# Kernel optimization log

Hardware: AMD Instinct MI355X
Metric: run time of the kernel (lower is better)

## Reference

```python
import jax, jax.numpy as jnp
import numpy as np

B, S, D = 2, 2048, 1024
H = 16
HD = D // H  # 64
THETA = 10000.0


def apply_rope(x, positions, theta):
    # x: (b, h, s, hd); positions: (s,)
    hd = x.shape[-1]
    inv_freq = theta ** (-jnp.arange(0, hd, 2, dtype=jnp.float32) / hd)  # (hd/2,)
    angles = positions.astype(jnp.float32)[:, None] * inv_freq[None, :]  # (s, hd/2)
    cos, sin = jnp.cos(angles), jnp.sin(angles)
    x1 = x[..., 0::2]
    x2 = x[..., 1::2]
    r1 = x1 * cos - x2 * sin
    r2 = x1 * sin + x2 * cos
    out = jnp.stack([r1, r2], axis=-1).reshape(x.shape)
    return out.astype(x.dtype)


def setup_inputs() -> dict:
    key = jax.random.key(0)
    ks = jax.random.split(key, 5)
    scale = 1.0 / np.sqrt(D)
    return {
        "in_features": jax.random.normal(ks[0], (B, S, D), dtype=jnp.float32),
        "token_positions": jnp.arange(S, dtype=jnp.int32),
        "Wq": jax.random.normal(ks[1], (D, D), dtype=jnp.float32) * scale,
        "Wk": jax.random.normal(ks[2], (D, D), dtype=jnp.float32) * scale,
        "Wv": jax.random.normal(ks[3], (D, D), dtype=jnp.float32) * scale,
        "Wo": jax.random.normal(ks[4], (D, D), dtype=jnp.float32) * scale,
    }


def reference(in_features, token_positions, Wq, Wk, Wv, Wo):
    b, s, d = in_features.shape
    h, hd = H, HD
    # bias-free linear: y = x @ W.T  (W is (out, in))
    q = in_features @ Wq.T
    k = in_features @ Wk.T
    v = in_features @ Wv.T
    # (b, s, h*hd) -> (b, h, s, hd)
    split = lambda t: t.reshape(b, s, h, hd).transpose(0, 2, 1, 3)
    q, k, v = split(q), split(k), split(v)
    q = apply_rope(q, token_positions, THETA)
    k = apply_rope(k, token_positions, THETA)
    scores = jnp.einsum("bhid,bhjd->bhij", q, k) / jnp.sqrt(jnp.asarray(hd, dtype=q.dtype))
    causal = jnp.triu(jnp.ones((s, s), dtype=bool), k=1)
    scores = jnp.where(causal, -jnp.inf, scores)
    attn = jax.nn.softmax(scores, axis=-1)
    out = jnp.einsum("bhij,bhjd->bhid", attn, v)
    out = out.transpose(0, 2, 1, 3).reshape(b, s, d)
    return out @ Wo.T
```

## Files before the change

kernel.cpp:

```cpp
#include <hip/hip_runtime.h>
#include <math.h>

#define NUM_HEADS 16
#define HEAD_DIM 64

typedef __bf16 bf16x8 __attribute__((ext_vector_type(8)));
typedef short shortx4 __attribute__((ext_vector_type(4)));
typedef float floatx4 __attribute__((ext_vector_type(4)));

__device__ __forceinline__ unsigned short f2b(float f) {
  unsigned int u = __float_as_uint(f);
  u += 0x7fffu + ((u >> 16) & 1u);
  return (unsigned short)(u >> 16);
}

__device__ __forceinline__ void async16(const void* g, void* l) {
  __builtin_amdgcn_global_load_lds(
      (const __attribute__((address_space(1))) unsigned int*)g,
      (__attribute__((address_space(3))) unsigned int*)l, 16, 0, 0);
}

__device__ __forceinline__ void cvt4(const float* in, unsigned short* out, int i) {
  float4 v = ((const float4*)in)[i];
  ushort4 o;
  o.x = f2b(v.x); o.y = f2b(v.y); o.z = f2b(v.z); o.w = f2b(v.w);
  ((ushort4*)out)[i] = o;
}

__global__ void prep(const float* __restrict__ x,
                     const float* __restrict__ w0, const float* __restrict__ w1,
                     const float* __restrict__ w2, const float* __restrict__ w3,
                     const int* __restrict__ pos,
                     unsigned short* Xb, unsigned short* o0, unsigned short* o1,
                     unsigned short* o2, unsigned short* o3,
                     float* __restrict__ tab, int xq, int w4, int ntab) {
  int i = blockIdx.x * 256 + threadIdx.x;
  int z = blockIdx.y;
  if (z == 0) {
    if (i < xq) {
#pragma unroll
      for (int rep = 0; rep < 4; ++rep) cvt4(x, Xb, rep * xq + i);
    }
  } else if (z <= 4) {
    if (i < w4) {
      const float* in = (z == 1) ? w0 : (z == 2) ? w1 : (z == 3) ? w2 : w3;
      unsigned short* out = (z == 1) ? o0 : (z == 2) ? o1 : (z == 3) ? o2 : o3;
      cvt4(in, out, i);
    }
  } else {
    if (i < ntab) {
      int fi = i & 31, s = i >> 5;
      float inv = expf(-0.28782313662425575f * (float)fi);
      float ang = (float)pos[s] * inv;
      float sn, cs;
      sincosf(ang, &sn, &cs);
      tab[i * 2] = cs;
      tab[i * 2 + 1] = sn;
    }
  }
}

template <int MODE, int MT>
__global__ __launch_bounds__(256, MODE == 1 ? 4 : 2)
void gemm_bt(const unsigned short* __restrict__ A,
             const unsigned short* __restrict__ B0,
             const unsigned short* __restrict__ B1,
             const unsigned short* __restrict__ B2,
             void* out0v, void* out1v, void* out2v,
             const float* __restrict__ ctab,
             int M, int N, int K, int S) {
  __shared__ unsigned short As[(MT / 16) * 512];
  __shared__ unsigned short Bs[8 * 512];
  const int tid = threadIdx.x;
  const int lane = tid & 63;
  const int w = tid >> 6;
  const int lane16 = lane & 15;
  const int g = lane >> 4;
  const int wm = w >> 1, wn = w & 1;
  const int m0 = blockIdx.y * MT;
  const int n0 = blockIdx.x * 128;
  const unsigned short* Bp = (blockIdx.z == 0) ? B0 : (blockIdx.z == 1 ? B1 : B2);
  constexpr int MTILES = MT / 32;

  const floatx4 vzero = {0.f, 0.f, 0.f, 0.f};
  floatx4 acc[MTILES][4];
#pragma unroll
  for (int i = 0; i < MTILES; i++)
#pragma unroll
    for (int j = 0; j < 4; j++) acc[i][j] = vzero;

  const int ar = lane >> 2;
  const int ac = (lane & 3) * 8;

  for (int k0 = 0; k0 < K; k0 += 32) {
    if constexpr (MT == 128) {
#pragma unroll
      for (int c = 0; c < 2; c++) {
        int chunk = w * 2 + c;
        async16(A  + (size_t)(m0 + chunk * 16 + ar) * K + k0 + ac, As + chunk * 512);
        async16(Bp + (size_t)(n0 + chunk * 16 + ar) * K + k0 + ac, Bs + chunk * 512);
      }
    } else {
      async16(A  + (size_t)(m0 + w * 16 + ar) * K + k0 + ac, As + w * 512);
      async16(Bp + (size_t)(n0 + w * 16 + ar) * K + k0 + ac, Bs + w * 512);
      async16(Bp + (size_t)(n0 + (w + 4) * 16 + ar) * K + k0 + ac, Bs + (w + 4) * 512);
    }
    __syncthreads();
    bf16x8 a[MTILES], b[4];
#pragma unroll
    for (int mt = 0; mt < MTILES; mt++)
      a[mt] = *(const bf16x8*)&As[(wm * (MT / 2) + mt * 16 + lane16) * 32 + g * 8];
#pragma unroll
    for (int nt = 0; nt < 4; nt++)
      b[nt] = *(const bf16x8*)&Bs[(wn * 64 + nt * 16 + lane16) * 32 + g * 8];
#pragma unroll
    for (int mt = 0; mt < MTILES; mt++)
#pragma unroll
      for (int nt = 0; nt < 4; nt++)
        acc[mt][nt] = __builtin_amdgcn_mfma_f32_16x16x32_bf16(b[nt], a[mt], acc[mt][nt], 0, 0, 0);
    __syncthreads();
  }

  if (MODE == 0) {
    if (blockIdx.z < 2) {
      unsigned short* outp = (unsigned short*)((blockIdx.z == 0) ? out0v : out1v);
      const float qs = (blockIdx.z == 0) ? 0.125f : 1.0f;
#pragma unroll
      for (int mt = 0; mt < MTILES; mt++) {
        int m = m0 + wm * (MT / 2) + mt * 16 + lane16;
        int bb = m / S, s = m - bb * S;
        const float* crow = ctab + (size_t)s * 64;
#pragma unroll
        for (int nt = 0; nt < 4; nt++) {
          int n = n0 + wn * 64 + nt * 16 + g * 4;
          int h = n >> 6, dl = n & 63;
          floatx4 v = acc[mt][nt];
          float4 cs = *(const float4*)&crow[dl];
          float r0 = (v[0] * cs.x - v[1] * cs.y) * qs;
          float r1 = (v[0] * cs.y + v[1] * cs.x) * qs;
          float r2 = (v[2] * cs.z - v[3] * cs.w) * qs;
          float r3 = (v[2] * cs.w + v[3] * cs.z) * qs;
          shortx4 st;
          st[0] = (short)f2b(r0); st[1] = (short)f2b(r1);
          st[2] = (short)f2b(r2); st[3] = (short)f2b(r3);
          *(shortx4*)&outp[(((size_t)(bb * NUM_HEADS + h) * S + s) << 6) + dl] = st;
        }
      }
    } else {
      unsigned short* outp = (unsigned short*)out2v;
#pragma unroll
      for (int mt = 0; mt < MTILES; mt++) {
        int m = m0 + wm * (MT / 2) + mt * 16 + lane16;
        int bb = m / S, s = m - bb * S;
#pragma unroll
        for (int nt = 0; nt < 4; nt++) {
          int n = n0 + wn * 64 + nt * 16 + g * 4;
          int bh = bb * NUM_HEADS + (n >> 6);
          int dl = n & 63;
          size_t dbase = ((size_t)bh * 64 + dl) * S + s;
#pragma unroll
          for (int r = 0; r < 4; r++)
            outp[dbase + (size_t)r * S] = f2b(acc[mt][nt][r]);
        }
      }
    }
  } else {
    float* outp = (float*)out0v;
#pragma unroll
    for (int mt = 0; mt < MTILES; mt++) {
      int m = m0 + wm * (MT / 2) + mt * 16 + lane16;
#pragma unroll
      for (int nt = 0; nt < 4; nt++) {
        int n = n0 + wn * 64 + nt * 16 + g * 4;
        *(floatx4*)&outp[(size_t)m * N + n] = acc[mt][nt];
      }
    }
  }
}

__global__ __launch_bounds__(256, 4)
void flash_attn4(const unsigned short* __restrict__ Q,
                 const unsigned short* __restrict__ Kv,
                 const unsigned short* __restrict__ Vt,
                 unsigned short* __restrict__ Oattn, int S) {
  __shared__ unsigned short Ks[2 * 4096];
  __shared__ unsigned short Vs[2 * 4096];
  const int tid = threadIdx.x;
  const int lane = tid & 63;
  const int w = tid >> 6;
  const int lane16 = lane & 15;
  const int g = lane >> 4;
  const int sw = lane16 & 7;
  const int qt = gridDim.x - 1 - blockIdx.x;
  const int bh = blockIdx.y;
  const int b = bh >> 4, h = bh & 15;
  const size_t kbase = (size_t)bh * S * HEAD_DIM;
  const unsigned short* Kbase = Kv + kbase;
  const unsigned short* Vtbase = Vt + (size_t)bh * HEAD_DIM * S;
  const int qrow0 = qt * 64 + w * 16;

  bf16x8 qf0, qf1;
  {
    const unsigned short* qp = Q + kbase + (size_t)(qrow0 + lane16) * HEAD_DIM + g * 8;
    qf0 = *(const bf16x8*)qp;
    qf1 = *(const bf16x8*)(qp + 32);
  }

  const int ci0 = w * 64 + lane;
  const int ci1 = ci0 + 256;
  const int r0 = ci0 >> 3, j0 = (ci0 & 7) ^ (r0 & 7);
  const int r1 = ci1 >> 3, j1 = (ci1 & 7) ^ (r1 & 7);
  const unsigned short* kS0 = Kbase + r0 * HEAD_DIM + j0 * 8;
  const unsigned short* kS1 = Kbase + r1 * HEAD_DIM + j1 * 8;
  const unsigned short* vS0 = Vtbase + (size_t)r0 * S + j0 * 8;
  const unsigned short* vS1 = Vtbase + (size_t)r1 * S + j1 * 8;
  unsigned short* kD0 = Ks + ci0 * 8;
  unsigned short* kD1 = Ks + ci1 * 8;
  unsigned short* vD0 = Vs + ci0 * 8;
  unsigned short* vD1 = Vs + ci1 * 8;

  auto stage = [&](int t, int bi) {
    int koff = t * 4096;
    int voff = t * 64;
    int doff = bi * 4096;
    async16(kS0 + koff, kD0 + doff);
    async16(kS1 + koff, kD1 + doff);
    async16(vS0 + voff, vD0 + doff);
    async16(vS1 + voff, vD1 + doff);
  };

  const floatx4 vzero = {0.f, 0.f, 0.f, 0.f};
  floatx4 oacc[4];
#pragma unroll
  for (int i = 0; i < 4; i++) oacc[i] = vzero;
  float l_i = 0.f;

  stage(0, 0);
  __syncthreads();

  for (int t = 0; t <= qt; ++t) {
    const int bi = t & 1;
    if (t < qt) stage(t + 1, bi ^ 1);
    const unsigned short* Kb_ = Ks + bi * 4096;
    const unsigned short* Vb_ = Vs + bi * 4096;

    floatx4 sc[4];
#pragma unroll
    for (int c = 0; c < 4; ++c) {
      int r = c * 16 + lane16;
      bf16x8 kf0 = *(const bf16x8*)&Kb_[(r * 8 + (g ^ sw)) * 8];
      bf16x8 kf1 = *(const bf16x8*)&Kb_[(r * 8 + ((4 + g) ^ sw)) * 8];
      floatx4 s = vzero;
      s = __builtin_amdgcn_mfma_f32_16x16x32_bf16(kf0, qf0, s, 0, 0, 0);
      s = __builtin_amdgcn_mfma_f32_16x16x32_bf16(kf1, qf1, s, 0, 0, 0);
      sc[c] = s;
    }
    if (t == qt) {
      const int i = qrow0 + lane16;
      const int jb = t * 64;
#pragma unroll
      for (int c = 0; c < 4; ++c)
#pragma unroll
        for (int r = 0; r < 4; ++r)
          if (jb + c * 16 + g * 4 + r > i) sc[c][r] = -INFINITY;
    }
    shortx4 pc[4];
#pragma unroll
    for (int c = 0; c < 4; ++c) {
      float p0 = __expf(sc[c][0]);
      float p1 = __expf(sc[c][1]);
      float p2 = __expf(sc[c][2]);
      float p3 = __expf(sc[c][3]);
      l_i += (p0 + p1) + (p2 + p3);
      union { unsigned int u[2]; shortx4 s4; } pu;
      pu.u[0] = __builtin_amdgcn_perm(__float_as_uint(p1), __float_as_uint(p0), 0x07060302u);
      pu.u[1] = __builtin_amdgcn_perm(__float_as_uint(p3), __float_as_uint(p2), 0x07060302u);
      pc[c] = pu.s4;
    }
#pragma unroll
    for (int nt = 0; nt < 4; ++nt) {
      int rv = nt * 16 + lane16;
#pragma unroll
      for (int c = 0; c < 4; ++c) {
        shortx4 vf = *(const shortx4*)&Vb_[(rv * 8 + ((c * 2 + (g >> 1)) ^ sw)) * 8 + (g & 1) * 4];
        oacc[nt] = __builtin_amdgcn_mfma_f32_16x16x16bf16_1k(vf, pc[c], oacc[nt], 0, 0, 0);
      }
    }
    __syncthreads();
  }

  l_i += __shfl_xor(l_i, 16, 64);
  l_i += __shfl_xor(l_i, 32, 64);
  {
    float inv = 1.0f / l_i;
    int srow = qrow0 + lane16;
    size_t rowb = ((size_t)b * S + srow) * 1024 + h * 64;
#pragma unroll
    for (int nt = 0; nt < 4; ++nt) {
      shortx4 st;
#pragma unroll
      for (int r = 0; r < 4; ++r) st[r] = (short)f2b(oacc[nt][r] * inv);
      *(shortx4*)&Oattn[rowb + nt * 16 + g * 4] = st;
    }
  }
}

extern "C" void kernel_launch(void* const* d_in, const int* in_sizes, int n_in,
                              void* d_out, int out_size, void* d_ws, size_t ws_size,
                              hipStream_t stream) {
  const float* x  = (const float*)d_in[0];
  const int*  pos = (const int*)d_in[1];
  const float* wq = (const float*)d_in[2];
  const float* wk = (const float*)d_in[3];
  const float* wv = (const float*)d_in[4];
  const float* wo = (const float*)d_in[5];

  const int D = 1024;
  const int S = in_sizes[1];
  const int M = in_sizes[0] / D;
  const int B = M / S;
  const int BH = B * NUM_HEADS;

  char* wsb = (char*)d_ws;
  size_t off = 0;
  auto alloc = [&](size_t bytes) {
    char* p = wsb + off;
    off += (bytes + 255) & ~(size_t)255;
    return p;
  };
  unsigned short* Xb   = (unsigned short*)alloc((size_t)M * D * 2);
  unsigned short* Wqb  = (unsigned short*)alloc((size_t)D * D * 2);
  unsigned short* Wkb  = (unsigned short*)alloc((size_t)D * D * 2);
  unsigned short* Wvb  = (unsigned short*)alloc((size_t)D * D * 2);
  unsigned short* Wob  = (unsigned short*)alloc((size_t)D * D * 2);
  unsigned short* Qb   = (unsigned short*)alloc((size_t)M * D * 2);
  unsigned short* Kb   = (unsigned short*)alloc((size_t)M * D * 2);
  unsigned short* Vtb  = (unsigned short*)alloc((size_t)M * D * 2);
  unsigned short* Attn = (unsigned short*)alloc((size_t)M * D * 2);
  float*          Ctab = (float*)alloc((size_t)S * 32 * 2 * 4);
  (void)ws_size;

  {
    int n4x = M * D / 4;
    int xq = n4x / 4;
    int w4 = D * D / 4;
    int ntab = S * 32;
    int gx = (w4 + 255) / 256;
    prep<<<dim3(gx, 6), 256, 0, stream>>>(x, wq, wk, wv, wo, pos,
                                          Xb, Wqb, Wkb, Wvb, Wob, Ctab,
                                          xq, w4, ntab);
  }
  gemm_bt<0, 128><<<dim3(D / 128, M / 128, 3), 256, 0, stream>>>(
      Xb, Wqb, Wkb, Wvb, Qb, Kb, Vtb, Ctab, M, D, D, S);
  flash_attn4<<<dim3(S / 64, BH), 256, 0, stream>>>(Qb, Kb, Vtb, Attn, S);
  gemm_bt<1, 64><<<dim3(D / 128, M / 64, 1), 256, 0, stream>>>(
      Attn, Wob, Wob, Wob, d_out, d_out, d_out, Ctab, M, D, D, S);
}
```

Baseline: 191.3 us.

## Pair complementary causal query tiles per block and use exp2 with folded scale

Each attention block now processes two query tiles, qa and NT-1-qa, sharing staged K/V tiles, which halves the grid and balances causal work across blocks. The softmax exponent switches to exp2, with log2(e) folded into the Q projection scale. Register pressure rises because two sets of accumulators are live, and launch bounds drop to 2 blocks per CU to allow for that.

```diff
diff --git a/kernel.cpp b/kernel.cpp
--- a/kernel.cpp
+++ b/kernel.cpp
@@ -7,6 +7,12 @@
 typedef __bf16 bf16x8 __attribute__((ext_vector_type(8)));
 typedef short shortx4 __attribute__((ext_vector_type(4)));
 typedef float floatx4 __attribute__((ext_vector_type(4)));
+
+#if __has_builtin(__builtin_amdgcn_exp2f)
+#define EXP2(x) __builtin_amdgcn_exp2f(x)
+#else
+#define EXP2(x) exp2f(x)
+#endif
 
 __device__ __forceinline__ unsigned short f2b(float f) {
   unsigned int u = __float_as_uint(f);
@@ -124,7 +130,7 @@
   if (MODE == 0) {
     if (blockIdx.z < 2) {
       unsigned short* outp = (unsigned short*)((blockIdx.z == 0) ? out0v : out1v);
-      const float qs = (blockIdx.z == 0) ? 0.125f : 1.0f;
+      const float qs = (blockIdx.z == 0) ? 0.18033688011112042f : 1.0f;
 #pragma unroll
       for (int mt = 0; mt < MTILES; mt++) {
         int m = m0 + wm * (MT / 2) + mt * 16 + lane16;
@@ -178,8 +184,8 @@
   }
 }
 
-__global__ __launch_bounds__(256, 4)
-void flash_attn4(const unsigned short* __restrict__ Q,
+__global__ __launch_bounds__(256, 2)
+void flash_attn5(const unsigned short* __restrict__ Q,
                  const unsigned short* __restrict__ Kv,
                  const unsigned short* __restrict__ Vt,
                  unsigned short* __restrict__ Oattn, int S) {
@@ -191,19 +197,25 @@
   const int lane16 = lane & 15;
   const int g = lane >> 4;
   const int sw = lane16 & 7;
-  const int qt = gridDim.x - 1 - blockIdx.x;
+  const int NT = S >> 6;
+  const int qa = blockIdx.x;
+  const int qb = NT - 1 - qa;
   const int bh = blockIdx.y;
   const int b = bh >> 4, h = bh & 15;
   const size_t kbase = (size_t)bh * S * HEAD_DIM;
   const unsigned short* Kbase = Kv + kbase;
   const unsigned short* Vtbase = Vt + (size_t)bh * HEAD_DIM * S;
-  const int qrow0 = qt * 64 + w * 16;
-
-  bf16x8 qf0, qf1;
+  const int qrowA = qa * 64 + w * 16;
+  const int qrowB = qb * 64 + w * 16;
+
+  bf16x8 qA0, qA1, qB0, qB1;
   {
-    const unsigned short* qp = Q + kbase + (size_t)(qrow0 + lane16) * HEAD_DIM + g * 8;
-    qf0 = *(const bf16x8*)qp;
-    qf1 = *(const bf16x8*)(qp + 32);
+    const unsigned short* qp = Q + kbase + (size_t)(qrowA + lane16) * HEAD_DIM + g * 8;
+    qA0 = *(const bf16x8*)qp;
+    qA1 = *(const bf16x8*)(qp + 32);
+    qp = Q + kbase + (size_t)(qrowB + lane16) * HEAD_DIM + g * 8;
+    qB0 = *(const bf16x8*)qp;
+    qB1 = *(const bf16x8*)(qp + 32);
   }
 
   const int ci0 = w * 64 + lane;
@@ -230,76 +242,141 @@
   };
 
   const floatx4 vzero = {0.f, 0.f, 0.f, 0.f};
-  floatx4 oacc[4];
-#pragma unroll
-  for (int i = 0; i < 4; i++) oacc[i] = vzero;
-  float l_i = 0.f;
+  floatx4 oA[4], oB[4];
+#pragma unroll
+  for (int i = 0; i < 4; i++) { oA[i] = vzero; oB[i] = vzero; }
+  float lA = 0.f, lB = 0.f;
 
   stage(0, 0);
   __syncthreads();
 
-  for (int t = 0; t <= qt; ++t) {
+  for (int t = 0; t <= qb; ++t) {
     const int bi = t & 1;
-    if (t < qt) stage(t + 1, bi ^ 1);
+    if (t < qb) stage(t + 1, bi ^ 1);
     const unsigned short* Kb_ = Ks + bi * 4096;
     const unsigned short* Vb_ = Vs + bi * 4096;
-
-    floatx4 sc[4];
+    const bool doA = (t <= qa);
+
+    bf16x8 kf0[4], kf1[4];
 #pragma unroll
     for (int c = 0; c < 4; ++c) {
       int r = c * 16 + lane16;
-      bf16x8 kf0 = *(const bf16x8*)&Kb_[(r * 8 + (g ^ sw)) * 8];
-      bf16x8 kf1 = *(const bf16x8*)&Kb_[(r * 8 + ((4 + g) ^ sw)) * 8];
+      kf0[c] = *(const bf16x8*)&Kb_[(r * 8 + (g ^ sw)) * 8];
+      kf1[c] = *(const bf16x8*)&Kb_[(r * 8 + ((4 + g) ^ sw)) * 8];
+    }
+
+    floatx4 scB[4];
+#pragma unroll
+    for (int c = 0; c < 4; ++c) {
       floatx4 s = vzero;
-      s = __builtin_amdgcn_mfma_f32_16x16x32_bf16(kf0, qf0, s, 0, 0, 0);
-      s = __builtin_amdgcn_mfma_f32_16x16x32_bf16(kf1, qf1, s, 0, 0, 0);
-      sc[c] = s;
-    }
-    if (t == qt) {
-      const int i = qrow0 + lane16;
+      s = __builtin_amdgcn_mfma_f32_16x16x32_bf16(kf0[c], qB0, s, 0, 0, 0);
+      s = __builtin_amdgcn_mfma_f32_16x16x32_bf16(kf1[c], qB1, s, 0, 0, 0);
+      scB[c] = s;
+    }
+    if (t == qb) {
+      const int i = qrowB + lane16;
       const int jb = t * 64;
 #pragma unroll
       for (int c = 0; c < 4; ++c)
 #pragma unroll
         for (int r = 0; r < 4; ++r)
-          if (jb + c * 16 + g * 4 + r > i) sc[c][r] = -INFINITY;
-    }
-    shortx4 pc[4];
+          if (jb + c * 16 + g * 4 + r > i) scB[c][r] = -INFINITY;
+    }
+    shortx4 pcB[4], pcA[4];
 #pragma unroll
     for (int c = 0; c < 4; ++c) {
-      float p0 = __expf(sc[c][0]);
-      float p1 = __expf(sc[c][1]);
-      float p2 = __expf(sc[c][2]);
-      float p3 = __expf(sc[c][3]);
-      l_i += (p0 + p1) + (p2 + p3);
+      float p0 = EXP2(scB[c][0]);
+      float p1 = EXP2(scB[c][1]);
+      float p2 = EXP2(scB[c][2]);
+      float p3 = EXP2(scB[c][3]);
+      lB += (p0 + p1) + (p2 + p3);
       union { unsigned int u[2]; shortx4 s4; } pu;
       pu.u[0] = __builtin_amdgcn_perm(__float_as_uint(p1), __float_as_uint(p0), 0x07060302u);
       pu.u[1] = __builtin_amdgcn_perm(__float_as_uint(p3), __float_as_uint(p2), 0x07060302u);
-      pc[c] = pu.s4;
-    }
-#pragma unroll
-    for (int nt = 0; nt < 4; ++nt) {
-      int rv = nt * 16 + lane16;
+      pcB[c] = pu.s4;
+    }
+
+    if (doA) {
+      floatx4 scA[4];
 #pragma unroll
       for (int c = 0; c < 4; ++c) {
-        shortx4 vf = *(const shortx4*)&Vb_[(rv * 8 + ((c * 2 + (g >> 1)) ^ sw)) * 8 + (g & 1) * 4];
-        oacc[nt] = __builtin_amdgcn_mfma_f32_16x16x16bf16_1k(vf, pc[c], oacc[nt], 0, 0, 0);
+        floatx4 s = vzero;
+        s = __builtin_amdgcn_mfma_f32_16x16x32_bf16(kf0[c], qA0, s, 0, 0, 0);
+        s = __builtin_amdgcn_mfma_f32_16x16x32_bf16(kf1[c], qA1, s, 0, 0, 0);
+        scA[c] = s;
+      }
+      if (t == qa) {
+        const int i = qrowA + lane16;
+        const int jb = t * 64;
+#pragma unroll
+        for (int c = 0; c < 4; ++c)
+#pragma unroll
+          for (int r = 0; r < 4; ++r)
+            if (jb + c * 16 + g * 4 + r > i) scA[c][r] = -INFINITY;
+      }
+#pragma unroll
+      for (int c = 0; c < 4; ++c) {
+        float p0 = EXP2(scA[c][0]);
+        float p1 = EXP2(scA[c][1]);
+        float p2 = EXP2(scA[c][2]);
+        float p3 = EXP2(scA[c][3]);
+        lA += (p0 + p1) + (p2 + p3);
+        union { unsigned int u[2]; shortx4 s4; } pu;
+        pu.u[0] = __builtin_amdgcn_perm(__float_as_uint(p1), __float_as_uint(p0), 0x07060302u);
+        pu.u[1] = __builtin_amdgcn_perm(__float_as_uint(p3), __float_as_uint(p2), 0x07060302u);
+        pcA[c] = pu.s4;
+      }
+#pragma unroll
+      for (int nt = 0; nt < 4; ++nt) {
+        int rv = nt * 16 + lane16;
+#pragma unroll
+        for (int c = 0; c < 4; ++c) {
+          shortx4 vf = *(const shortx4*)&Vb_[(rv * 8 + ((c * 2 + (g >> 1)) ^ sw)) * 8 + (g & 1) * 4];
+          oB[nt] = __builtin_amdgcn_mfma_f32_16x16x16bf16_1k(vf, pcB[c], oB[nt], 0, 0, 0);
+          oA[nt] = __builtin_amdgcn_mfma_f32_16x16x16bf16_1k(vf, pcA[c], oA[nt], 0, 0, 0);
+        }
+      }
+    } else {
+#pragma unroll
+      for (int nt = 0; nt < 4; ++nt) {
+        int rv = nt * 16 + lane16;
+#pragma unroll
+        for (int c = 0; c < 4; ++c) {
+          shortx4 vf = *(const shortx4*)&Vb_[(rv * 8 + ((c * 2 + (g >> 1)) ^ sw)) * 8 + (g & 1) * 4];
+          oB[nt] = __builtin_amdgcn_mfma_f32_16x16x16bf16_1k(vf, pcB[c], oB[nt], 0, 0, 0);
+        }
       }
     }
     __syncthreads();
   }
 
-  l_i += __shfl_xor(l_i, 16, 64);
-  l_i += __shfl_xor(l_i, 32, 64);
   {
-    float inv = 1.0f / l_i;
-    int srow = qrow0 + lane16;
+    float l = lA;
+    l += __shfl_xor(l, 16, 64);
+    l += __shfl_xor(l, 32, 64);
+    float inv = 1.0f / l;
+    int srow = qrowA + lane16;
     size_t rowb = ((size_t)b * S + srow) * 1024 + h * 64;
 #pragma unroll
     for (int nt = 0; nt < 4; ++nt) {
       shortx4 st;
 #pragma unroll
-      for (int r = 0; r < 4; ++r) st[r] = (short)f2b(oacc[nt][r] * inv);
+      for (int r = 0; r < 4; ++r) st[r] = (short)f2b(oA[nt][r] * inv);
+      *(shortx4*)&Oattn[rowb + nt * 16 + g * 4] = st;
+    }
+  }
+  {
+    float l = lB;
+    l += __shfl_xor(l, 16, 64);
+    l += __shfl_xor(l, 32, 64);
+    float inv = 1.0f / l;
+    int srow = qrowB + lane16;
+    size_t rowb = ((size_t)b * S + srow) * 1024 + h * 64;
+#pragma unroll
+    for (int nt = 0; nt < 4; ++nt) {
+      shortx4 st;
+#pragma unroll
+      for (int r = 0; r < 4; ++r) st[r] = (short)f2b(oB[nt][r] * inv);
       *(shortx4*)&Oattn[rowb + nt * 16 + g * 4] = st;
     }
   }
@@ -352,7 +429,7 @@
   }
   gemm_bt<0, 128><<<dim3(D / 128, M / 128, 3), 256, 0, stream>>>(
       Xb, Wqb, Wkb, Wvb, Qb, Kb, Vtb, Ctab, M, D, D, S);
-  flash_attn4<<<dim3(S / 64, BH), 256, 0, stream>>>(Qb, Kb, Vtb, Attn, S);
+  flash_attn5<<<dim3(S / 128, BH), 256, 0, stream>>>(Qb, Kb, Vtb, Attn, S);
   gemm_bt<1, 64><<<dim3(D / 128, M / 64, 1), 256, 0, stream>>>(
       Attn, Wob, Wob, Wob, d_out, d_out, d_out, Ctab, M, D, D, S);
 }
```

Result: faster. 181.0 us (-5.4%).

## Pair mirrored causal query tiles per block and fold log2e into Q scale

Applied to the files above, without the earlier changes.

The flash attention kernel now runs 512 threads per block. Each block processes two query tiles, qa and its mirror NT-1-qa, so every block does the same total causal work. The shared K/V tiles are staged once for both halves, and waves stop computing once they pass their own diagonal tile. The Q scale now includes log2(e), so exp2 replaces expf. In exchange, the half of the block assigned to the short tile sits idle at barriers, and occupancy at 512 threads may be lower.

```diff
diff --git a/kernel.cpp b/kernel.cpp
--- a/kernel.cpp
+++ b/kernel.cpp
@@ -7,6 +7,12 @@
 typedef __bf16 bf16x8 __attribute__((ext_vector_type(8)));
 typedef short shortx4 __attribute__((ext_vector_type(4)));
 typedef float floatx4 __attribute__((ext_vector_type(4)));
+
+#if __has_builtin(__builtin_amdgcn_exp2f)
+#define EXP2(x) __builtin_amdgcn_exp2f(x)
+#else
+#define EXP2(x) exp2f(x)
+#endif
 
 __device__ __forceinline__ unsigned short f2b(float f) {
   unsigned int u = __float_as_uint(f);
@@ -124,7 +130,7 @@
   if (MODE == 0) {
     if (blockIdx.z < 2) {
       unsigned short* outp = (unsigned short*)((blockIdx.z == 0) ? out0v : out1v);
-      const float qs = (blockIdx.z == 0) ? 0.125f : 1.0f;
+      const float qs = (blockIdx.z == 0) ? 0.18033688011112042f : 1.0f;
 #pragma unroll
       for (int mt = 0; mt < MTILES; mt++) {
         int m = m0 + wm * (MT / 2) + mt * 16 + lane16;
@@ -178,8 +184,8 @@
   }
 }
 
-__global__ __launch_bounds__(256, 4)
-void flash_attn4(const unsigned short* __restrict__ Q,
+__global__ __launch_bounds__(512, 4)
+void flash_attn6(const unsigned short* __restrict__ Q,
                  const unsigned short* __restrict__ Kv,
                  const unsigned short* __restrict__ Vt,
                  unsigned short* __restrict__ Oattn, int S) {
@@ -191,13 +197,17 @@
   const int lane16 = lane & 15;
   const int g = lane >> 4;
   const int sw = lane16 & 7;
-  const int qt = gridDim.x - 1 - blockIdx.x;
+  const int NT = S >> 6;
+  const int qa = blockIdx.x;
+  const int qb = NT - 1 - qa;
+  const int myq = (w & 4) ? qb : qa;
+  const int wq = w & 3;
   const int bh = blockIdx.y;
   const int b = bh >> 4, h = bh & 15;
   const size_t kbase = (size_t)bh * S * HEAD_DIM;
   const unsigned short* Kbase = Kv + kbase;
   const unsigned short* Vtbase = Vt + (size_t)bh * HEAD_DIM * S;
-  const int qrow0 = qt * 64 + w * 16;
+  const int qrow0 = myq * 64 + wq * 16;
 
   bf16x8 qf0, qf1;
   {
@@ -206,27 +216,17 @@
     qf1 = *(const bf16x8*)(qp + 32);
   }
 
-  const int ci0 = w * 64 + lane;
-  const int ci1 = ci0 + 256;
-  const int r0 = ci0 >> 3, j0 = (ci0 & 7) ^ (r0 & 7);
-  const int r1 = ci1 >> 3, j1 = (ci1 & 7) ^ (r1 & 7);
-  const unsigned short* kS0 = Kbase + r0 * HEAD_DIM + j0 * 8;
-  const unsigned short* kS1 = Kbase + r1 * HEAD_DIM + j1 * 8;
-  const unsigned short* vS0 = Vtbase + (size_t)r0 * S + j0 * 8;
-  const unsigned short* vS1 = Vtbase + (size_t)r1 * S + j1 * 8;
-  unsigned short* kD0 = Ks + ci0 * 8;
-  unsigned short* kD1 = Ks + ci1 * 8;
-  unsigned short* vD0 = Vs + ci0 * 8;
-  unsigned short* vD1 = Vs + ci1 * 8;
+  const int ci = tid;
+  const int r = ci >> 3, j = (ci & 7) ^ (r & 7);
+  const unsigned short* kS = Kbase + r * HEAD_DIM + j * 8;
+  const unsigned short* vS = Vtbase + (size_t)r * S + j * 8;
+  unsigned short* kD = Ks + ci * 8;
+  unsigned short* vD = Vs + ci * 8;
 
   auto stage = [&](int t, int bi) {
-    int koff = t * 4096;
-    int voff = t * 64;
     int doff = bi * 4096;
-    async16(kS0 + koff, kD0 + doff);
-    async16(kS1 + koff, kD1 + doff);
-    async16(vS0 + voff, vD0 + doff);
-    async16(vS1 + voff, vD1 + doff);
+    async16(kS + t * 4096, kD + doff);
+    async16(vS + t * 64, vD + doff);
   };
 
   const floatx4 vzero = {0.f, 0.f, 0.f, 0.f};
@@ -238,52 +238,54 @@
   stage(0, 0);
   __syncthreads();
 
-  for (int t = 0; t <= qt; ++t) {
+  for (int t = 0; t <= qb; ++t) {
     const int bi = t & 1;
-    if (t < qt) stage(t + 1, bi ^ 1);
-    const unsigned short* Kb_ = Ks + bi * 4096;
-    const unsigned short* Vb_ = Vs + bi * 4096;
-
-    floatx4 sc[4];
-#pragma unroll
-    for (int c = 0; c < 4; ++c) {
-      int r = c * 16 + lane16;
-      bf16x8 kf0 = *(const bf16x8*)&Kb_[(r * 8 + (g ^ sw)) * 8];
-      bf16x8 kf1 = *(const bf16x8*)&Kb_[(r * 8 + ((4 + g) ^ sw)) * 8];
-      floatx4 s = vzero;
-      s = __builtin_amdgcn_mfma_f32_16x16x32_bf16(kf0, qf0, s, 0, 0, 0);
-      s = __builtin_amdgcn_mfma_f32_16x16x32_bf16(kf1, qf1, s, 0, 0, 0);
-      sc[c] = s;
-    }
-    if (t == qt) {
-      const int i = qrow0 + lane16;
-      const int jb = t * 64;
-#pragma unroll
-      for (int c = 0; c < 4; ++c)
-#pragma unroll
-        for (int r = 0; r < 4; ++r)
-          if (jb + c * 16 + g * 4 + r > i) sc[c][r] = -INFINITY;
-    }
-    shortx4 pc[4];
-#pragma unroll
-    for (int c = 0; c < 4; ++c) {
-      float p0 = __expf(sc[c][0]);
-      float p1 = __expf(sc[c][1]);
-      float p2 = __expf(sc[c][2]);
-      float p3 = __expf(sc[c][3]);
-      l_i += (p0 + p1) + (p2 + p3);
-      union { unsigned int u[2]; shortx4 s4; } pu;
-      pu.u[0] = __builtin_amdgcn_perm(__float_as_uint(p1), __float_as_uint(p0), 0x07060302u);
-      pu.u[1] = __builtin_amdgcn_perm(__float_as_uint(p3), __float_as_uint(p2), 0x07060302u);
-      pc[c] = pu.s4;
-    }
-#pragma unroll
-    for (int nt = 0; nt < 4; ++nt) {
-      int rv = nt * 16 + lane16;
+    if (t < qb) stage(t + 1, bi ^ 1);
+    if (t <= myq) {
+      const unsigned short* Kb_ = Ks + bi * 4096;
+      const unsigned short* Vb_ = Vs + bi * 4096;
+
+      floatx4 sc[4];
 #pragma unroll
       for (int c = 0; c < 4; ++c) {
-        shortx4 vf = *(const shortx4*)&Vb_[(rv * 8 + ((c * 2 + (g >> 1)) ^ sw)) * 8 + (g & 1) * 4];
-        oacc[nt] = __builtin_amdgcn_mfma_f32_16x16x16bf16_1k(vf, pc[c], oacc[nt], 0, 0, 0);
+        int rr = c * 16 + lane16;
+        bf16x8 kf0 = *(const bf16x8*)&Kb_[(rr * 8 + (g ^ sw)) * 8];
+        bf16x8 kf1 = *(const bf16x8*)&Kb_[(rr * 8 + ((4 + g) ^ sw)) * 8];
+        floatx4 s = vzero;
+        s = __builtin_amdgcn_mfma_f32_16x16x32_bf16(kf0, qf0, s, 0, 0, 0);
+        s = __builtin_amdgcn_mfma_f32_16x16x32_bf16(kf1, qf1, s, 0, 0, 0);
+        sc[c] = s;
+      }
+      if (t == myq) {
+        const int i = qrow0 + lane16;
+        const int jb = t * 64;
+#pragma unroll
+        for (int c = 0; c < 4; ++c)
+#pragma unroll
+          for (int rr = 0; rr < 4; ++rr)
+            if (jb + c * 16 + g * 4 + rr > i) sc[c][rr] = -INFINITY;
+      }
+      shortx4 pc[4];
+#pragma unroll
+      for (int c = 0; c < 4; ++c) {
+        float p0 = EXP2(sc[c][0]);
+        float p1 = EXP2(sc[c][1]);
+        float p2 = EXP2(sc[c][2]);
+        float p3 = EXP2(sc[c][3]);
+        l_i += (p0 + p1) + (p2 + p3);
+        union { unsigned int u[2]; shortx4 s4; } pu;
+        pu.u[0] = __builtin_amdgcn_perm(__float_as_uint(p1), __float_as_uint(p0), 0x07060302u);
+        pu.u[1] = __builtin_amdgcn_perm(__float_as_uint(p3), __float_as_uint(p2), 0x07060302u);
+        pc[c] = pu.s4;
+      }
+#pragma unroll
+      for (int nt = 0; nt < 4; ++nt) {
+        int rv = nt * 16 + lane16;
+#pragma unroll
+        for (int c = 0; c < 4; ++c) {
+          shortx4 vf = *(const shortx4*)&Vb_[(rv * 8 + ((c * 2 + (g >> 1)) ^ sw)) * 8 + (g & 1) * 4];
+          oacc[nt] = __builtin_amdgcn_mfma_f32_16x16x16bf16_1k(vf, pc[c], oacc[nt], 0, 0, 0);
+        }
       }
     }
     __syncthreads();
@@ -299,7 +301,7 @@
     for (int nt = 0; nt < 4; ++nt) {
       shortx4 st;
 #pragma unroll
-      for (int r = 0; r < 4; ++r) st[r] = (short)f2b(oacc[nt][r] * inv);
+      for (int rr = 0; rr < 4; ++rr) st[rr] = (short)f2b(oacc[nt][rr] * inv);
       *(shortx4*)&Oattn[rowb + nt * 16 + g * 4] = st;
     }
   }
@@ -352,7 +354,7 @@
   }
   gemm_bt<0, 128><<<dim3(D / 128, M / 128, 3), 256, 0, stream>>>(
       Xb, Wqb, Wkb, Wvb, Qb, Kb, Vtb, Ctab, M, D, D, S);
-  flash_attn4<<<dim3(S / 64, BH), 256, 0, stream>>>(Qb, Kb, Vtb, Attn, S);
+  flash_attn6<<<dim3(S / 128, BH), 512, 0, stream>>>(Qb, Kb, Vtb, Attn, S);
   gemm_bt<1, 64><<<dim3(D / 128, M / 64, 1), 256, 0, stream>>>(
       Attn, Wob, Wob, Wob, d_out, d_out, d_out, Ctab, M, D, D, S);
 }
```

Result: faster. 185.7 us (-3.0%).
